# Performance work log

Measured on AMD Instinct MI355X. Metric: run time of the kernel, lower is better.

## Reference

```python
import jax, jax.numpy as jnp
import numpy as np
import math

B, T, D, H = 2, 2048, 1024, 16
DH = D // H

def setup_inputs() -> dict:
    key = jax.random.key(0)
    ks = jax.random.split(key, 7)
    s = 0.02
    return {
        "q": jax.random.normal(ks[0], (B, T, D), jnp.float32),
        "k": jax.random.normal(ks[1], (B, T, D), jnp.float32),
        "v": jax.random.normal(ks[2], (B, T, D), jnp.float32),
        "wq": jax.random.normal(ks[3], (D, D), jnp.float32) * s,
        "wk": jax.random.normal(ks[4], (D, D), jnp.float32) * s,
        "wv": jax.random.normal(ks[5], (D, D), jnp.float32) * s,
        "wo": jax.random.normal(ks[6], (D, D), jnp.float32) * s,
    }

def reference(q, k, v, wq, wk, wv, wo):
    # nn.Linear(bias=False): y = x @ W.T
    qh = (q @ wq.T).reshape(B, T, H, DH).transpose(0, 2, 1, 3)  # [B,H,T,DH]
    kh = (k @ wk.T).reshape(B, T, H, DH).transpose(0, 2, 1, 3)
    vh = (v @ wv.T).reshape(B, T, H, DH).transpose(0, 2, 1, 3)
    scores = jnp.einsum('bhqd,bhkd->bhqk', qh, kh) / math.sqrt(DH)
    # causal mask: disallow j > i
    mask = jnp.triu(jnp.ones((T, T), dtype=bool), k=1)
    scores = jnp.where(mask[None, None], -jnp.inf, scores)
    attn = jax.nn.softmax(scores, axis=-1)  # dropout=0 (eval)
    out = jnp.einsum('bhqk,bhkd->bhqd', attn, vh)
    out = out.transpose(0, 2, 1, 3).reshape(B, T, D)
    return out @ wo.T
```

## Files before the change

### kernel.cpp

```cpp
#include <hip/hip_runtime.h>
#include <cstdint>
#include <cstddef>

#define B_  2
#define T_  2048
#define D_  1024
#define H_  16
#define DH_ 64
#define M_  (B_*T_)

typedef __bf16 bf16x8 __attribute__((ext_vector_type(8)));
typedef float  f32x4  __attribute__((ext_vector_type(4)));
typedef unsigned short us4 __attribute__((ext_vector_type(4)));
typedef unsigned short us8 __attribute__((ext_vector_type(8)));
typedef unsigned short ushort_t;

__device__ __forceinline__ unsigned short f32_to_bf16_rne(float f) {
    unsigned u = __builtin_bit_cast(unsigned, f);
    u += 0x7FFFu + ((u >> 16) & 1u);
    return (unsigned short)(u >> 16);
}

__device__ __forceinline__ void async16(const void* g, void* l) {
    __builtin_amdgcn_global_load_lds(
        (const __attribute__((address_space(1))) unsigned int*)(uintptr_t)g,
        (__attribute__((address_space(3))) unsigned int*)(uintptr_t)l, 16, 0, 0);
}

__global__ __launch_bounds__(256) void cvt_all(
    const float* __restrict__ i0, const float* __restrict__ i1, const float* __restrict__ i2,
    const float* __restrict__ i3, const float* __restrict__ i4, const float* __restrict__ i5,
    const float* __restrict__ i6,
    ushort_t* __restrict__ o0, ushort_t* __restrict__ o1, ushort_t* __restrict__ o2,
    ushort_t* __restrict__ o3, ushort_t* __restrict__ o4, ushort_t* __restrict__ o5,
    ushort_t* __restrict__ o6) {
    const int y = blockIdx.y;
    const float* in = y == 0 ? i0 : y == 1 ? i1 : y == 2 ? i2 : y == 3 ? i3
                    : y == 4 ? i4 : y == 5 ? i5 : i6;
    ushort_t* out  = y == 0 ? o0 : y == 1 ? o1 : y == 2 ? o2 : y == 3 ? o3
                    : y == 4 ? o4 : y == 5 ? o5 : o6;
    const int n = (y < 3) ? (M_ * D_) : (D_ * D_);
    int i = (blockIdx.x * 256 + threadIdx.x) * 4;
    if (i >= n) return;
    float4 f = *reinterpret_cast<const float4*>(in + i);
    us4 o;
    o[0] = f32_to_bf16_rne(f.x); o[1] = f32_to_bf16_rne(f.y);
    o[2] = f32_to_bf16_rne(f.z); o[3] = f32_to_bf16_rne(f.w);
    *reinterpret_cast<us4*>(out + i) = o;
}

__device__ __forceinline__ void gemm_mainloop(const ushort_t* __restrict__ A,
                                              const ushort_t* __restrict__ W,
                                              ushort_t* As, ushort_t* Bs,
                                              int m0, int n0, f32x4 acc[4][4]) {
    const int tid  = threadIdx.x;
    const int lc   = tid & 15;
    const int quad = (tid >> 4) & 3;
    const int wave = tid >> 6;
    const int wm = (wave >> 1) * 64, wn = (wave & 1) * 64;
    const int sw = lc & 7;

    const f32x4 fzero = {0.f, 0.f, 0.f, 0.f};
#pragma unroll
    for (int mt = 0; mt < 4; ++mt)
#pragma unroll
        for (int nt = 0; nt < 4; ++nt) acc[mt][nt] = fzero;

    for (int kk = 0; kk < D_; kk += 64) {
        __syncthreads();
#pragma unroll
        for (int i = 0; i < 4; ++i) {
            const int j = i * 256 + tid;
            const int r = j >> 3, c = (j & 7) ^ (r & 7);
            async16(A + (size_t)(m0 + r) * D_ + kk + c * 8, As + j * 8);
            async16(W + (size_t)(n0 + r) * D_ + kk + c * 8, Bs + j * 8);
        }
        __syncthreads();
#pragma unroll
        for (int ks = 0; ks < 2; ++ks) {
            bf16x8 af[4], bw[4];
#pragma unroll
            for (int mt = 0; mt < 4; ++mt)
                af[mt] = *reinterpret_cast<const bf16x8*>(
                    As + (wm + mt * 16 + lc) * 64 + (((ks * 4 + quad) ^ sw) * 8));
#pragma unroll
            for (int nt = 0; nt < 4; ++nt)
                bw[nt] = *reinterpret_cast<const bf16x8*>(
                    Bs + (wn + nt * 16 + lc) * 64 + (((ks * 4 + quad) ^ sw) * 8));
#pragma unroll
            for (int mt = 0; mt < 4; ++mt)
#pragma unroll
                for (int nt = 0; nt < 4; ++nt)
                    acc[mt][nt] = __builtin_amdgcn_mfma_f32_16x16x32_bf16(af[mt], bw[nt], acc[mt][nt], 0, 0, 0);
        }
    }
}

__global__ __launch_bounds__(256, 3) void gemm_qkv(
    const ushort_t* __restrict__ qb, const ushort_t* __restrict__ kb, const ushort_t* __restrict__ vb,
    const ushort_t* __restrict__ wqb, const ushort_t* __restrict__ wkb, const ushort_t* __restrict__ wvb,
    ushort_t* __restrict__ qhb, ushort_t* __restrict__ khb, ushort_t* __restrict__ vtb) {
    __shared__ __align__(16) ushort_t As[128 * 64];
    __shared__ __align__(16) ushort_t Bs[128 * 64];
    __shared__ __align__(16) ushort_t Ts[4][64 * 16];

    const int z = blockIdx.z;
    const ushort_t* A = z == 0 ? qb : z == 1 ? kb : vb;
    const ushort_t* W = z == 0 ? wqb : z == 1 ? wkb : wvb;
    const int m0 = blockIdx.y * 128, n0 = blockIdx.x * 128;

    f32x4 acc[4][4];
    gemm_mainloop(A, W, As, Bs, m0, n0, acc);

    const int tid = threadIdx.x, lane = tid & 63, lc = tid & 15;
    const int quad = (tid >> 4) & 3, wave = tid >> 6;
    const int wm = (wave >> 1) * 64, wn = (wave & 1) * 64;

    if (z < 2) {
        ushort_t* outp = z == 0 ? qhb : khb;
#pragma unroll
        for (int mt = 0; mt < 4; ++mt)
#pragma unroll
            for (int nt = 0; nt < 4; ++nt)
#pragma unroll
                for (int r = 0; r < 4; ++r) {
                    const int m = m0 + wm + mt * 16 + quad * 4 + r;
                    const int n = n0 + wn + nt * 16 + lc;
                    const int bb = m >> 11, t = m & (T_ - 1);
                    const int hh = n >> 6,  d = n & 63;
                    outp[(((size_t)bb * H_ + hh) * T_ + t) * DH_ + d] = f32_to_bf16_rne(acc[mt][nt][r]);
                }
    } else {
        const int mG = m0 + wm;
        const int bb = mG >> 11, t0 = mG & (T_ - 1);
        const int nG = n0 + wn, hh = nG >> 6;
        ushort_t* base = vtb + ((size_t)bb * H_ + hh) * DH_ * T_;
#pragma unroll
        for (int mt = 0; mt < 4; ++mt) {
#pragma unroll
            for (int nt = 0; nt < 4; ++nt)
#pragma unroll
                for (int r = 0; r < 4; ++r)
                    Ts[wave][(nt * 16 + lc) * 16 + quad * 4 + r] = f32_to_bf16_rne(acc[mt][nt][r]);
#pragma unroll
            for (int it = 0; it < 2; ++it) {
                const int c = it * 64 + lane;
                const int nl = c >> 1, mh = c & 1;
                us8 vv = *reinterpret_cast<const us8*>(Ts[wave] + c * 8);
                *reinterpret_cast<us8*>(base + (size_t)nl * T_ + t0 + mt * 16 + mh * 8) = vv;
            }
        }
    }
}

__global__ __launch_bounds__(256, 3) void gemm_wo(const ushort_t* __restrict__ A,
                                                  const ushort_t* __restrict__ W,
                                                  float* __restrict__ out) {
    __shared__ __align__(16) ushort_t As[128 * 64];
    __shared__ __align__(16) ushort_t Bs[128 * 64];
    const int m0 = blockIdx.y * 128, n0 = blockIdx.x * 128;
    f32x4 acc[4][4];
    gemm_mainloop(A, W, As, Bs, m0, n0, acc);

    const int tid = threadIdx.x, lc = tid & 15;
    const int quad = (tid >> 4) & 3, wave = tid >> 6;
    const int wm = (wave >> 1) * 64, wn = (wave & 1) * 64;
#pragma unroll
    for (int mt = 0; mt < 4; ++mt)
#pragma unroll
        for (int nt = 0; nt < 4; ++nt)
#pragma unroll
            for (int r = 0; r < 4; ++r) {
                const int m = m0 + wm + mt * 16 + quad * 4 + r;
                const int n = n0 + wn + nt * 16 + lc;
                out[(size_t)m * D_ + n] = acc[mt][nt][r];
            }
}

__global__ __launch_bounds__(512, 4) void attn3(const ushort_t* __restrict__ Qh,
                                                const ushort_t* __restrict__ Kh,
                                                const ushort_t* __restrict__ Vt,
                                                ushort_t* __restrict__ Ao) {
    __shared__ __align__(16) ushort_t smem[40960];

    const int tid = threadIdx.x, lane = tid & 63, lc = tid & 15;
    const int quad = (tid >> 4) & 3, wave = tid >> 6;
    const int grp = wave >> 2, sub = wave & 3;
    const int sw = lc & 7;
    const int bh = blockIdx.y, bb = bh >> 4, hh = bh & 15;

    const ushort_t* Qp = Qh + (size_t)bh * T_ * DH_;
    const ushort_t* Kp = Kh + (size_t)bh * T_ * DH_;
    const ushort_t* Vp = Vt + (size_t)bh * DH_ * T_;
    const float SC2 = 0.18033688f;
    const f32x4 fzero = {0.f, 0.f, 0.f, 0.f};

    ushort_t* Pw = smem + 32768 + wave * 1024;

    for (int pass = 0; pass < 2; ++pass) {
        const int qt = pass ? (31 - (int)blockIdx.x) : (int)blockIdx.x;
        const int q0 = qt * 64, nkt = qt + 1;
        const int nIt = (nkt + 1) >> 1;
        const int mbase = q0 + sub * 16;

        const ushort_t* qrow = Qp + (size_t)(mbase + lc) * DH_ + quad * 8;
        bf16x8 aq0 = *reinterpret_cast<const bf16x8*>(qrow);
        bf16x8 aq1 = *reinterpret_cast<const bf16x8*>(qrow + 32);

        f32x4 o[4];
        float lsum[4];
#pragma unroll
        for (int ct = 0; ct < 4; ++ct) o[ct] = fzero;
#pragma unroll
        for (int r = 0; r < 4; ++r) lsum[r] = 0.f;

        auto stagePair = [&](int buf, int kt0) {
            const int l = tid, r = l >> 3, c = (l & 7) ^ (r & 7);
            ushort_t* Kd0 = smem + (buf * 2 + 0) * 4096;
            ushort_t* Kd1 = smem + (buf * 2 + 1) * 4096;
            ushort_t* Vd0 = smem + 16384 + (buf * 2 + 0) * 4096;
            ushort_t* Vd1 = smem + 16384 + (buf * 2 + 1) * 4096;
            if (kt0 < nkt)     async16(Kp + (size_t)(kt0 * 64 + r) * DH_ + c * 8,       Kd0 + l * 8);
            if (kt0 + 1 < nkt) async16(Kp + (size_t)((kt0 + 1) * 64 + r) * DH_ + c * 8, Kd1 + l * 8);
            if (kt0 < nkt)     async16(Vp + (size_t)r * T_ + kt0 * 64 + c * 8,          Vd0 + l * 8);
            if (kt0 + 1 < nkt) async16(Vp + (size_t)r * T_ + (kt0 + 1) * 64 + c * 8,    Vd1 + l * 8);
        };

        __syncthreads();
        stagePair(0, 0);

        for (int it = 0; it < nIt; ++it) {
            const int buf = it & 1;
            __syncthreads();
            if (it + 1 < nIt) stagePair(buf ^ 1, 2 * (it + 1));

            const int kt = 2 * it + grp;
            if (kt < nkt) {
                const int k0 = kt * 64;
                const ushort_t* Kt = smem + (buf * 2 + grp) * 4096;
                const ushort_t* Vtile = smem + 16384 + (buf * 2 + grp) * 4096;

                f32x4 s[4];
#pragma unroll
                for (int ct = 0; ct < 4; ++ct) {
                    const ushort_t* kr = Kt + (ct * 16 + lc) * 64;
                    bf16x8 bk0 = *reinterpret_cast<const bf16x8*>(kr + ((quad ^ sw) * 8));
                    bf16x8 bk1 = *reinterpret_cast<const bf16x8*>(kr + (((4 + quad) ^ sw) * 8));
                    s[ct] = __builtin_amdgcn_mfma_f32_16x16x32_bf16(aq0, bk0, fzero, 0, 0, 0);
                    s[ct] = __builtin_amdgcn_mfma_f32_16x16x32_bf16(aq1, bk1, s[ct], 0, 0, 0);
                }

#pragma unroll
                for (int ct = 0; ct < 4; ++ct) {
                    const int col = k0 + ct * 16 + lc;
#pragma unroll
                    for (int r = 0; r < 4; ++r) {
                        const int row = mbase + quad * 4 + r;
                        const float e = (col <= row) ? __builtin_amdgcn_exp2f(s[ct][r] * SC2) : 0.f;
                        lsum[r] += e;
                        const int prow = quad * 4 + r, pcol = ct * 16 + lc;
                        Pw[prow * 64 + (((pcol >> 3) ^ (prow & 7)) * 8) + (pcol & 7)] = f32_to_bf16_rne(e);
                    }
                }
                bf16x8 ap0 = *reinterpret_cast<const bf16x8*>(Pw + lc * 64 + ((quad ^ sw) * 8));
                bf16x8 ap1 = *reinterpret_cast<const bf16x8*>(Pw + lc * 64 + (((4 + quad) ^ sw) * 8));

#pragma unroll
                for (int ct = 0; ct < 4; ++ct) {
                    const ushort_t* vr = Vtile + (ct * 16 + lc) * 64;
                    bf16x8 bv0 = *reinterpret_cast<const bf16x8*>(vr + ((quad ^ sw) * 8));
                    bf16x8 bv1 = *reinterpret_cast<const bf16x8*>(vr + (((4 + quad) ^ sw) * 8));
                    o[ct] = __builtin_amdgcn_mfma_f32_16x16x32_bf16(ap0, bv0, o[ct], 0, 0, 0);
                    o[ct] = __builtin_amdgcn_mfma_f32_16x16x32_bf16(ap1, bv1, o[ct], 0, 0, 0);
                }
            }
        }

        __syncthreads();
        float* Osh = (float*)smem;
        float* Lsh = (float*)(smem + 16384);
        if (grp == 0) {
#pragma unroll
            for (int ct = 0; ct < 4; ++ct)
#pragma unroll
                for (int r = 0; r < 4; ++r)
                    Osh[sub * 1024 + (quad * 4 + r) * 64 + ct * 16 + lc] = o[ct][r];
#pragma unroll
            for (int r = 0; r < 4; ++r) Lsh[sub * 256 + lane * 4 + r] = lsum[r];
        }
        __syncthreads();
        if (grp == 1) {
            float inv[4];
#pragma unroll
            for (int r = 0; r < 4; ++r) {
                float l = lsum[r] + Lsh[sub * 256 + lane * 4 + r];
#pragma unroll
                for (int d = 1; d < 16; d <<= 1) l += __shfl_xor(l, d);
                inv[r] = 1.0f / l;
            }
#pragma unroll
            for (int ct = 0; ct < 4; ++ct)
#pragma unroll
                for (int r = 0; r < 4; ++r) {
                    const float ov = o[ct][r] + Osh[sub * 1024 + (quad * 4 + r) * 64 + ct * 16 + lc];
                    const int rowq = mbase + quad * 4 + r;
                    Ao[((size_t)bb * T_ + rowq) * D_ + hh * DH_ + ct * 16 + lc] =
                        f32_to_bf16_rne(ov * inv[r]);
                }
        }
    }
}

extern "C" void kernel_launch(void* const* d_in, const int* in_sizes, int n_in,
                              void* d_out, int out_size, void* d_ws, size_t ws_size,
                              hipStream_t stream) {
    const float* q  = (const float*)d_in[0];
    const float* k  = (const float*)d_in[1];
    const float* v  = (const float*)d_in[2];
    const float* wq = (const float*)d_in[3];
    const float* wk = (const float*)d_in[4];
    const float* wv = (const float*)d_in[5];
    const float* wo = (const float*)d_in[6];

    char* ws = (char*)d_ws;
    size_t off = 0;
    auto alloc = [&](size_t bytes) -> char* {
        char* p = ws + off;
        off += (bytes + 255) & ~(size_t)255;
        return p;
    };
    ushort_t* qb  = (ushort_t*)alloc((size_t)M_ * D_ * 2);
    ushort_t* kb  = (ushort_t*)alloc((size_t)M_ * D_ * 2);
    ushort_t* vb  = (ushort_t*)alloc((size_t)M_ * D_ * 2);
    ushort_t* wqb = (ushort_t*)alloc((size_t)D_ * D_ * 2);
    ushort_t* wkb = (ushort_t*)alloc((size_t)D_ * D_ * 2);
    ushort_t* wvb = (ushort_t*)alloc((size_t)D_ * D_ * 2);
    ushort_t* wob = (ushort_t*)alloc((size_t)D_ * D_ * 2);
    ushort_t* qhb = (ushort_t*)alloc((size_t)M_ * D_ * 2);
    ushort_t* khb = (ushort_t*)alloc((size_t)M_ * D_ * 2);
    ushort_t* vtb = (ushort_t*)alloc((size_t)M_ * D_ * 2);
    ushort_t* aob = (ushort_t*)alloc((size_t)M_ * D_ * 2);

    cvt_all<<<dim3(4096, 7), 256, 0, stream>>>(q, k, v, wq, wk, wv, wo,
                                               qb, kb, vb, wqb, wkb, wvb, wob);

    gemm_qkv<<<dim3(8, 32, 3), 256, 0, stream>>>(qb, kb, vb, wqb, wkb, wvb, qhb, khb, vtb);

    attn3<<<dim3(16, 32), 512, 0, stream>>>(qhb, khb, vtb, aob);

    gemm_wo<<<dim3(8, 32), 256, 0, stream>>>(aob, wob, (float*)d_out);
}
```

Before: 209.1 us.

## Restructure attention to 2 row-tiles per wave, XCD-aware block remap, smaller Wo tiles

The attention kernel moves from 8 to 4 waves per block, and each wave now handles 32 query rows so the K and V fragments loaded from shared memory are reused twice. K rows are permuted at load time so each lane's scores map to contiguous P columns, which allows packed 4-wide P writes into a padded buffer. The causal mask is applied only on the diagonal tile, and blocks are remapped so heads group per XCD. The QKV GEMM epilogue is staged through LDS so Q and K outputs are written as 16-byte stores, and gemm_wo uses 64x128 tiles with a block swizzle for more blocks. The added register pressure and the halved block size could lower occupancy.

```diff
diff --git a/kernel.cpp b/kernel.cpp
--- a/kernel.cpp
+++ b/kernel.cpp
@@ -102,12 +102,14 @@
     ushort_t* __restrict__ qhb, ushort_t* __restrict__ khb, ushort_t* __restrict__ vtb) {
     __shared__ __align__(16) ushort_t As[128 * 64];
     __shared__ __align__(16) ushort_t Bs[128 * 64];
-    __shared__ __align__(16) ushort_t Ts[4][64 * 16];
+    __shared__ __align__(16) ushort_t Ts[4][16 * 80];
 
     const int z = blockIdx.z;
     const ushort_t* A = z == 0 ? qb : z == 1 ? kb : vb;
     const ushort_t* W = z == 0 ? wqb : z == 1 ? wkb : wvb;
-    const int m0 = blockIdx.y * 128, n0 = blockIdx.x * 128;
+    const int yt = blockIdx.x + 8 * (blockIdx.y >> 3);
+    const int xt = blockIdx.y & 7;
+    const int m0 = yt * 128, n0 = xt * 128;
 
     f32x4 acc[4][4];
     gemm_mainloop(A, W, As, Bs, m0, n0, acc);
@@ -115,25 +117,28 @@
     const int tid = threadIdx.x, lane = tid & 63, lc = tid & 15;
     const int quad = (tid >> 4) & 3, wave = tid >> 6;
     const int wm = (wave >> 1) * 64, wn = (wave & 1) * 64;
+    const int mG = m0 + wm;
+    const int bb = mG >> 11, t0 = mG & (T_ - 1);
+    const int hh = (n0 + wn) >> 6;
 
     if (z < 2) {
-        ushort_t* outp = z == 0 ? qhb : khb;
-#pragma unroll
-        for (int mt = 0; mt < 4; ++mt)
+        ushort_t* outp = (z == 0 ? qhb : khb) + ((size_t)bb * H_ + hh) * T_ * DH_;
+#pragma unroll
+        for (int mt = 0; mt < 4; ++mt) {
 #pragma unroll
             for (int nt = 0; nt < 4; ++nt)
 #pragma unroll
-                for (int r = 0; r < 4; ++r) {
-                    const int m = m0 + wm + mt * 16 + quad * 4 + r;
-                    const int n = n0 + wn + nt * 16 + lc;
-                    const int bb = m >> 11, t = m & (T_ - 1);
-                    const int hh = n >> 6,  d = n & 63;
-                    outp[(((size_t)bb * H_ + hh) * T_ + t) * DH_ + d] = f32_to_bf16_rne(acc[mt][nt][r]);
-                }
+                for (int r = 0; r < 4; ++r)
+                    Ts[wave][(quad * 4 + r) * 80 + nt * 16 + lc] = f32_to_bf16_rne(acc[mt][nt][r]);
+#pragma unroll
+            for (int it = 0; it < 2; ++it) {
+                const int c = it * 64 + lane;
+                const int row = c >> 3, c8 = c & 7;
+                us8 vv = *reinterpret_cast<const us8*>(Ts[wave] + row * 80 + c8 * 8);
+                *reinterpret_cast<us8*>(outp + (size_t)(t0 + mt * 16 + row) * DH_ + c8 * 8) = vv;
+            }
+        }
     } else {
-        const int mG = m0 + wm;
-        const int bb = mG >> 11, t0 = mG & (T_ - 1);
-        const int nG = n0 + wn, hh = nG >> 6;
         ushort_t* base = vtb + ((size_t)bb * H_ + hh) * DH_ * T_;
 #pragma unroll
         for (int mt = 0; mt < 4; ++mt) {
@@ -153,20 +158,63 @@
     }
 }
 
-__global__ __launch_bounds__(256, 3) void gemm_wo(const ushort_t* __restrict__ A,
+__global__ __launch_bounds__(256, 4) void gemm_wo(const ushort_t* __restrict__ A,
                                                   const ushort_t* __restrict__ W,
                                                   float* __restrict__ out) {
-    __shared__ __align__(16) ushort_t As[128 * 64];
+    __shared__ __align__(16) ushort_t As[64 * 64];
     __shared__ __align__(16) ushort_t Bs[128 * 64];
-    const int m0 = blockIdx.y * 128, n0 = blockIdx.x * 128;
-    f32x4 acc[4][4];
-    gemm_mainloop(A, W, As, Bs, m0, n0, acc);
+    const int yt = blockIdx.x + 8 * (blockIdx.y >> 3);
+    const int xt = blockIdx.y & 7;
+    const int m0 = yt * 64, n0 = xt * 128;
 
     const int tid = threadIdx.x, lc = tid & 15;
     const int quad = (tid >> 4) & 3, wave = tid >> 6;
-    const int wm = (wave >> 1) * 64, wn = (wave & 1) * 64;
-#pragma unroll
-    for (int mt = 0; mt < 4; ++mt)
+    const int wm = (wave >> 1) * 32, wn = (wave & 1) * 64;
+    const int sw = lc & 7;
+
+    const f32x4 fzero = {0.f, 0.f, 0.f, 0.f};
+    f32x4 acc[2][4];
+#pragma unroll
+    for (int mt = 0; mt < 2; ++mt)
+#pragma unroll
+        for (int nt = 0; nt < 4; ++nt) acc[mt][nt] = fzero;
+
+    for (int kk = 0; kk < D_; kk += 64) {
+        __syncthreads();
+#pragma unroll
+        for (int i = 0; i < 2; ++i) {
+            const int j = i * 256 + tid;
+            const int r = j >> 3, c = (j & 7) ^ (r & 7);
+            async16(A + (size_t)(m0 + r) * D_ + kk + c * 8, As + j * 8);
+        }
+#pragma unroll
+        for (int i = 0; i < 4; ++i) {
+            const int j = i * 256 + tid;
+            const int r = j >> 3, c = (j & 7) ^ (r & 7);
+            async16(W + (size_t)(n0 + r) * D_ + kk + c * 8, Bs + j * 8);
+        }
+        __syncthreads();
+#pragma unroll
+        for (int ks = 0; ks < 2; ++ks) {
+            bf16x8 af[2], bw[4];
+#pragma unroll
+            for (int mt = 0; mt < 2; ++mt)
+                af[mt] = *reinterpret_cast<const bf16x8*>(
+                    As + (wm + mt * 16 + lc) * 64 + (((ks * 4 + quad) ^ sw) * 8));
+#pragma unroll
+            for (int nt = 0; nt < 4; ++nt)
+                bw[nt] = *reinterpret_cast<const bf16x8*>(
+                    Bs + (wn + nt * 16 + lc) * 64 + (((ks * 4 + quad) ^ sw) * 8));
+#pragma unroll
+            for (int mt = 0; mt < 2; ++mt)
+#pragma unroll
+                for (int nt = 0; nt < 4; ++nt)
+                    acc[mt][nt] = __builtin_amdgcn_mfma_f32_16x16x32_bf16(af[mt], bw[nt], acc[mt][nt], 0, 0, 0);
+        }
+    }
+
+#pragma unroll
+    for (int mt = 0; mt < 2; ++mt)
 #pragma unroll
         for (int nt = 0; nt < 4; ++nt)
 #pragma unroll
@@ -177,17 +225,22 @@
             }
 }
 
-__global__ __launch_bounds__(512, 4) void attn3(const ushort_t* __restrict__ Qh,
+__global__ __launch_bounds__(256, 2) void attn4(const ushort_t* __restrict__ Qh,
                                                 const ushort_t* __restrict__ Kh,
                                                 const ushort_t* __restrict__ Vt,
                                                 ushort_t* __restrict__ Ao) {
-    __shared__ __align__(16) ushort_t smem[40960];
+    __shared__ __align__(16) ushort_t smem[32768 + 4 * 16 * 88];
 
     const int tid = threadIdx.x, lane = tid & 63, lc = tid & 15;
     const int quad = (tid >> 4) & 3, wave = tid >> 6;
-    const int grp = wave >> 2, sub = wave & 3;
+    const int grp = wave >> 1, sub = wave & 1;
     const int sw = lc & 7;
-    const int bh = blockIdx.y, bb = bh >> 4, hh = bh & 15;
+
+    const int L = blockIdx.x;
+    const int xcd = L & 7, slot = L >> 3;
+    const int bh = xcd + 8 * (slot >> 4);
+    const int xp = slot & 15;
+    const int bb = bh >> 4, hh = bh & 15;
 
     const ushort_t* Qp = Qh + (size_t)bh * T_ * DH_;
     const ushort_t* Kp = Kh + (size_t)bh * T_ * DH_;
@@ -195,35 +248,51 @@
     const float SC2 = 0.18033688f;
     const f32x4 fzero = {0.f, 0.f, 0.f, 0.f};
 
-    ushort_t* Pw = smem + 32768 + wave * 1024;
+    ushort_t* Pw = smem + 32768 + wave * (16 * 88);
 
     for (int pass = 0; pass < 2; ++pass) {
-        const int qt = pass ? (31 - (int)blockIdx.x) : (int)blockIdx.x;
+        const int qt = pass ? (31 - xp) : xp;
         const int q0 = qt * 64, nkt = qt + 1;
         const int nIt = (nkt + 1) >> 1;
-        const int mbase = q0 + sub * 16;
-
-        const ushort_t* qrow = Qp + (size_t)(mbase + lc) * DH_ + quad * 8;
-        bf16x8 aq0 = *reinterpret_cast<const bf16x8*>(qrow);
-        bf16x8 aq1 = *reinterpret_cast<const bf16x8*>(qrow + 32);
-
-        f32x4 o[4];
-        float lsum[4];
-#pragma unroll
-        for (int ct = 0; ct < 4; ++ct) o[ct] = fzero;
-#pragma unroll
-        for (int r = 0; r < 4; ++r) lsum[r] = 0.f;
+        const int mbase = q0 + sub * 32;
+
+        bf16x8 aq[2][2];
+#pragma unroll
+        for (int mt = 0; mt < 2; ++mt) {
+            const ushort_t* qrow = Qp + (size_t)(mbase + mt * 16 + lc) * DH_ + quad * 8;
+            aq[mt][0] = *reinterpret_cast<const bf16x8*>(qrow);
+            aq[mt][1] = *reinterpret_cast<const bf16x8*>(qrow + 32);
+        }
+
+        f32x4 o[2][4];
+        float lsum[2][4];
+#pragma unroll
+        for (int mt = 0; mt < 2; ++mt) {
+#pragma unroll
+            for (int ct = 0; ct < 4; ++ct) o[mt][ct] = fzero;
+#pragma unroll
+            for (int r = 0; r < 4; ++r) lsum[mt][r] = 0.f;
+        }
 
         auto stagePair = [&](int buf, int kt0) {
-            const int l = tid, r = l >> 3, c = (l & 7) ^ (r & 7);
-            ushort_t* Kd0 = smem + (buf * 2 + 0) * 4096;
-            ushort_t* Kd1 = smem + (buf * 2 + 1) * 4096;
-            ushort_t* Vd0 = smem + 16384 + (buf * 2 + 0) * 4096;
-            ushort_t* Vd1 = smem + 16384 + (buf * 2 + 1) * 4096;
-            if (kt0 < nkt)     async16(Kp + (size_t)(kt0 * 64 + r) * DH_ + c * 8,       Kd0 + l * 8);
-            if (kt0 + 1 < nkt) async16(Kp + (size_t)((kt0 + 1) * 64 + r) * DH_ + c * 8, Kd1 + l * 8);
-            if (kt0 < nkt)     async16(Vp + (size_t)r * T_ + kt0 * 64 + c * 8,          Vd0 + l * 8);
-            if (kt0 + 1 < nkt) async16(Vp + (size_t)r * T_ + (kt0 + 1) * 64 + c * 8,    Vd1 + l * 8);
+#pragma unroll
+            for (int i = 0; i < 2; ++i) {
+                const int j = i * 256 + tid;
+                const int r = j >> 3, c = (j & 7) ^ (r & 7);
+                const int kprm = 4 * (r & 15) + (r >> 4);
+                ushort_t* Kd0 = smem + (buf * 2 + 0) * 4096;
+                ushort_t* Kd1 = smem + (buf * 2 + 1) * 4096;
+                ushort_t* Vd0 = smem + 16384 + (buf * 2 + 0) * 4096;
+                ushort_t* Vd1 = smem + 16384 + (buf * 2 + 1) * 4096;
+                if (kt0 < nkt) {
+                    async16(Kp + (size_t)(kt0 * 64 + kprm) * DH_ + c * 8, Kd0 + j * 8);
+                    async16(Vp + (size_t)r * T_ + kt0 * 64 + c * 8,       Vd0 + j * 8);
+                }
+                if (kt0 + 1 < nkt) {
+                    async16(Kp + (size_t)((kt0 + 1) * 64 + kprm) * DH_ + c * 8, Kd1 + j * 8);
+                    async16(Vp + (size_t)r * T_ + (kt0 + 1) * 64 + c * 8,       Vd1 + j * 8);
+                }
+            }
         };
 
         __syncthreads();
@@ -237,41 +306,65 @@
             const int kt = 2 * it + grp;
             if (kt < nkt) {
                 const int k0 = kt * 64;
-                const ushort_t* Kt = smem + (buf * 2 + grp) * 4096;
+                const ushort_t* Kt    = smem + (buf * 2 + grp) * 4096;
                 const ushort_t* Vtile = smem + 16384 + (buf * 2 + grp) * 4096;
 
-                f32x4 s[4];
+                bf16x8 bv[4][2];
+#pragma unroll
+                for (int ct = 0; ct < 4; ++ct) {
+                    const ushort_t* vr = Vtile + (ct * 16 + lc) * 64;
+                    bv[ct][0] = *reinterpret_cast<const bf16x8*>(vr + ((quad ^ sw) * 8));
+                    bv[ct][1] = *reinterpret_cast<const bf16x8*>(vr + (((4 + quad) ^ sw) * 8));
+                }
+
+                f32x4 s[2][4];
 #pragma unroll
                 for (int ct = 0; ct < 4; ++ct) {
                     const ushort_t* kr = Kt + (ct * 16 + lc) * 64;
                     bf16x8 bk0 = *reinterpret_cast<const bf16x8*>(kr + ((quad ^ sw) * 8));
                     bf16x8 bk1 = *reinterpret_cast<const bf16x8*>(kr + (((4 + quad) ^ sw) * 8));
-                    s[ct] = __builtin_amdgcn_mfma_f32_16x16x32_bf16(aq0, bk0, fzero, 0, 0, 0);
-                    s[ct] = __builtin_amdgcn_mfma_f32_16x16x32_bf16(aq1, bk1, s[ct], 0, 0, 0);
-                }
-
-#pragma unroll
-                for (int ct = 0; ct < 4; ++ct) {
-                    const int col = k0 + ct * 16 + lc;
+#pragma unroll
+                    for (int mt = 0; mt < 2; ++mt) {
+                        s[mt][ct] = __builtin_amdgcn_mfma_f32_16x16x32_bf16(aq[mt][0], bk0, fzero, 0, 0, 0);
+                        s[mt][ct] = __builtin_amdgcn_mfma_f32_16x16x32_bf16(aq[mt][1], bk1, s[mt][ct], 0, 0, 0);
+                    }
+                }
+
+#pragma unroll
+                for (int mt = 0; mt < 2; ++mt) {
+                    float e[4][4];
+                    if (kt == qt) {
+#pragma unroll
+                        for (int ct = 0; ct < 4; ++ct) {
+                            const int key = k0 + 4 * lc + ct;
+#pragma unroll
+                            for (int r = 0; r < 4; ++r) {
+                                const int row = mbase + mt * 16 + quad * 4 + r;
+                                e[ct][r] = (key <= row) ? __builtin_amdgcn_exp2f(s[mt][ct][r] * SC2) : 0.f;
+                            }
+                        }
+                    } else {
+#pragma unroll
+                        for (int ct = 0; ct < 4; ++ct)
+#pragma unroll
+                            for (int r = 0; r < 4; ++r)
+                                e[ct][r] = __builtin_amdgcn_exp2f(s[mt][ct][r] * SC2);
+                    }
 #pragma unroll
                     for (int r = 0; r < 4; ++r) {
-                        const int row = mbase + quad * 4 + r;
-                        const float e = (col <= row) ? __builtin_amdgcn_exp2f(s[ct][r] * SC2) : 0.f;
-                        lsum[r] += e;
-                        const int prow = quad * 4 + r, pcol = ct * 16 + lc;
-                        Pw[prow * 64 + (((pcol >> 3) ^ (prow & 7)) * 8) + (pcol & 7)] = f32_to_bf16_rne(e);
+                        lsum[mt][r] += e[0][r] + e[1][r] + e[2][r] + e[3][r];
+                        us4 pk;
+                        pk[0] = f32_to_bf16_rne(e[0][r]); pk[1] = f32_to_bf16_rne(e[1][r]);
+                        pk[2] = f32_to_bf16_rne(e[2][r]); pk[3] = f32_to_bf16_rne(e[3][r]);
+                        *reinterpret_cast<us4*>(Pw + (quad * 4 + r) * 88 + lc * 4) = pk;
                     }
-                }
-                bf16x8 ap0 = *reinterpret_cast<const bf16x8*>(Pw + lc * 64 + ((quad ^ sw) * 8));
-                bf16x8 ap1 = *reinterpret_cast<const bf16x8*>(Pw + lc * 64 + (((4 + quad) ^ sw) * 8));
-
-#pragma unroll
-                for (int ct = 0; ct < 4; ++ct) {
-                    const ushort_t* vr = Vtile + (ct * 16 + lc) * 64;
-                    bf16x8 bv0 = *reinterpret_cast<const bf16x8*>(vr + ((quad ^ sw) * 8));
-                    bf16x8 bv1 = *reinterpret_cast<const bf16x8*>(vr + (((4 + quad) ^ sw) * 8));
-                    o[ct] = __builtin_amdgcn_mfma_f32_16x16x32_bf16(ap0, bv0, o[ct], 0, 0, 0);
-                    o[ct] = __builtin_amdgcn_mfma_f32_16x16x32_bf16(ap1, bv1, o[ct], 0, 0, 0);
+                    bf16x8 ap0 = *reinterpret_cast<const bf16x8*>(Pw + lc * 88 + quad * 8);
+                    bf16x8 ap1 = *reinterpret_cast<const bf16x8*>(Pw + lc * 88 + 32 + quad * 8);
+#pragma unroll
+                    for (int ct = 0; ct < 4; ++ct) {
+                        o[mt][ct] = __builtin_amdgcn_mfma_f32_16x16x32_bf16(ap0, bv[ct][0], o[mt][ct], 0, 0, 0);
+                        o[mt][ct] = __builtin_amdgcn_mfma_f32_16x16x32_bf16(ap1, bv[ct][1], o[mt][ct], 0, 0, 0);
+                    }
                 }
             }
         }
@@ -281,32 +374,40 @@
         float* Lsh = (float*)(smem + 16384);
         if (grp == 0) {
 #pragma unroll
-            for (int ct = 0; ct < 4; ++ct)
+            for (int mt = 0; mt < 2; ++mt) {
+#pragma unroll
+                for (int ct = 0; ct < 4; ++ct)
+#pragma unroll
+                    for (int r = 0; r < 4; ++r)
+                        Osh[(sub * 32 + mt * 16 + quad * 4 + r) * 64 + ct * 16 + lc] = o[mt][ct][r];
 #pragma unroll
                 for (int r = 0; r < 4; ++r)
-                    Osh[sub * 1024 + (quad * 4 + r) * 64 + ct * 16 + lc] = o[ct][r];
-#pragma unroll
-            for (int r = 0; r < 4; ++r) Lsh[sub * 256 + lane * 4 + r] = lsum[r];
+                    Lsh[(sub * 32 + mt * 16 + quad * 4 + r) * 16 + lc] = lsum[mt][r];
+            }
         }
         __syncthreads();
         if (grp == 1) {
-            float inv[4];
-#pragma unroll
-            for (int r = 0; r < 4; ++r) {
-                float l = lsum[r] + Lsh[sub * 256 + lane * 4 + r];
-#pragma unroll
-                for (int d = 1; d < 16; d <<= 1) l += __shfl_xor(l, d);
-                inv[r] = 1.0f / l;
-            }
-#pragma unroll
-            for (int ct = 0; ct < 4; ++ct)
+#pragma unroll
+            for (int mt = 0; mt < 2; ++mt) {
+                float inv[4];
 #pragma unroll
                 for (int r = 0; r < 4; ++r) {
-                    const float ov = o[ct][r] + Osh[sub * 1024 + (quad * 4 + r) * 64 + ct * 16 + lc];
-                    const int rowq = mbase + quad * 4 + r;
-                    Ao[((size_t)bb * T_ + rowq) * D_ + hh * DH_ + ct * 16 + lc] =
-                        f32_to_bf16_rne(ov * inv[r]);
-                }
+                    float l = lsum[mt][r] + Lsh[(sub * 32 + mt * 16 + quad * 4 + r) * 16 + lc];
+#pragma unroll
+                    for (int d = 1; d < 16; d <<= 1) l += __shfl_xor(l, d);
+                    inv[r] = 1.0f / l;
+                }
+#pragma unroll
+                for (int ct = 0; ct < 4; ++ct)
+#pragma unroll
+                    for (int r = 0; r < 4; ++r) {
+                        const int rowq = mbase + mt * 16 + quad * 4 + r;
+                        const float ov = o[mt][ct][r] +
+                            Osh[(sub * 32 + mt * 16 + quad * 4 + r) * 64 + ct * 16 + lc];
+                        Ao[((size_t)bb * T_ + rowq) * D_ + hh * DH_ + ct * 16 + lc] =
+                            f32_to_bf16_rne(ov * inv[r]);
+                    }
+            }
         }
     }
 }
@@ -346,7 +447,7 @@
 
     gemm_qkv<<<dim3(8, 32, 3), 256, 0, stream>>>(qb, kb, vb, wqb, wkb, wvb, qhb, khb, vtb);
 
-    attn3<<<dim3(16, 32), 512, 0, stream>>>(qhb, khb, vtb, aob);
-
-    gemm_wo<<<dim3(8, 32), 256, 0, stream>>>(aob, wob, (float*)d_out);
-}
+    attn4<<<dim3(512), 256, 0, stream>>>(qhb, khb, vtb, aob);
+
+    gemm_wo<<<dim3(8, 64), 256, 0, stream>>>(aob, wob, (float*)d_out);
+}
```

Result: faster. 197.9 us (-5.4%).
